# Kernel tuning notes

Hardware: AMD Instinct MI355X
Metric: run time of the kernel (lower is better)

The kernel has to match this reference:

```python
import jax, jax.numpy as jnp
import numpy as np

B, S, HID = 2, 2048, 2048
H, G = 32, 8            # query heads, kv heads
D = HID // H            # head_dim = 64
QPG = H // G            # q heads per kv group = 4


def setup_inputs() -> dict:
    key = jax.random.key(0)
    ks = jax.random.split(key, 5)
    sc = 0.02
    return {
        "x": jax.random.normal(ks[0], (B, S, HID), jnp.float32),
        "Wq": jax.random.normal(ks[1], (HID, HID), jnp.float32) * sc,
        "bq": jnp.zeros((HID,), jnp.float32),
        "Wk": jax.random.normal(ks[2], (HID, G * D), jnp.float32) * sc,
        "bk": jnp.zeros((G * D,), jnp.float32),
        "Wv": jax.random.normal(ks[3], (HID, G * D), jnp.float32) * sc,
        "bv": jnp.zeros((G * D,), jnp.float32),
        "Wo": jax.random.normal(ks[4], (HID, HID), jnp.float32) * sc,
        "bo": jnp.zeros((HID,), jnp.float32),
    }


def reference(x, Wq, bq, Wk, bk, Wv, bv, Wo, bo):
    b, s, _ = x.shape
    # projections (weights stored as [in, out])
    q = (x @ Wq + bq).reshape(b, s, G, QPG, D)      # [b,s,g,p,d]
    k = (x @ Wk + bk).reshape(b, s, G, D)           # [b,s,g,d]
    v = (x @ Wv + bv).reshape(b, s, G, D)
    scale = 1.0 / jnp.sqrt(jnp.asarray(D, x.dtype))
    # grouped attention: repeat_interleave of K/V expressed as shared g axis
    scores = jnp.einsum('bsgpd,btgd->bgpst', q, k) * scale  # [b,g,p,s,t]
    w = jax.nn.softmax(scores, axis=-1)
    o = jnp.einsum('bgpst,btgd->bsgpd', w, v)               # [b,s,g,p,d]
    o = o.reshape(b, s, HID)
    return o @ Wo + bo
```

## Files before the change

### kernel.cpp

```cpp
#include <hip/hip_runtime.h>
#include <hip/hip_bf16.h>


typedef __attribute__((ext_vector_type(8))) short shortx8;
typedef __attribute__((ext_vector_type(4))) float floatx4;

#define SEQ 2048
#define QSC 0.1803368801111204f

#if __has_builtin(__builtin_amdgcn_exp2f)
#define EXP2F(x) __builtin_amdgcn_exp2f(x)
#else
#define EXP2F(x) __expf((x) * 0.6931471805599453f)
#endif

__device__ __forceinline__ unsigned short f2bf(float f) {
  union { float f; unsigned u; } a; a.f = f;
  unsigned u = a.u;
  u += 0x7fffu + ((u >> 16) & 1u);
  return (unsigned short)(u >> 16);
}

__device__ __forceinline__ unsigned cvtpkbf(float lo, float hi) {
  unsigned r;
  asm("v_cvt_pk_bf16_f32 %0, %1, %2" : "=v"(r) : "v"(lo), "v"(hi));
  return r;
}

__device__ __forceinline__ void plswap(unsigned &a, unsigned &b) {
  asm("v_permlane32_swap_b32 %0, %1" : "+v"(a), "+v"(b));
}
__device__ __forceinline__ void pl16swap(unsigned &a, unsigned &b) {
  asm("v_permlane16_swap_b32 %0, %1" : "+v"(a), "+v"(b));
}

__device__ __forceinline__ void gload16(const unsigned short* g, unsigned short* l) {
  __builtin_amdgcn_global_load_lds((const __attribute__((address_space(1))) void*)g,
                                   (__attribute__((address_space(3))) void*)l, 16, 0, 0);
}

__global__ void prep_kernel(const float* __restrict__ x,
                            const float* __restrict__ Wq, const float* __restrict__ Wk,
                            const float* __restrict__ Wv, const float* __restrict__ Wo,
                            const float* __restrict__ bq, const float* __restrict__ bk,
                            const float* __restrict__ bv,
                            unsigned short* __restrict__ WT,
                            unsigned short* __restrict__ WoT,
                            unsigned short* __restrict__ xb,
                            float* __restrict__ bqkv) {
  const int z = blockIdx.z;
  if (z == 4) {
    int fb = blockIdx.y * 64 + blockIdx.x;
    int tid = threadIdx.y * 32 + threadIdx.x;
    int i = fb * 2048 + tid * 8;
    float4 v0 = *(const float4*)(x + i);
    float4 v1 = *(const float4*)(x + i + 4);
    ushort4 o0, o1;
    o0.x = f2bf(v0.x); o0.y = f2bf(v0.y); o0.z = f2bf(v0.z); o0.w = f2bf(v0.w);
    o1.x = f2bf(v1.x); o1.y = f2bf(v1.y); o1.z = f2bf(v1.z); o1.w = f2bf(v1.w);
    *(ushort4*)(xb + i) = o0;
    *(ushort4*)(xb + i + 4) = o1;
    return;
  }
  if (z == 5) {
    int fb = blockIdx.y * 64 + blockIdx.x;
    if (fb >= 12) return;
    int i = fb * 256 + threadIdx.y * 32 + threadIdx.x;
    if (i < 2048) bqkv[i] = bq[i] * QSC;
    else if (i < 2560) bqkv[i] = bk[i - 2048];
    else if (i < 3072) bqkv[i] = bv[i - 2560];
    return;
  }
  const float* W; unsigned short* D; int N; float sc = 1.f;
  if (z == 0)      { W = Wq; D = WT;               N = 2048; sc = QSC; }
  else if (z == 1) { W = Wk; D = WT + 2048 * 2048; N = 512; }
  else if (z == 2) { W = Wv; D = WT + 2560 * 2048; N = 512; }
  else             { W = Wo; D = WoT;              N = 2048; }
  if (blockIdx.x * 32 >= N) return;

  __shared__ float tile[32][33];
  int xx = blockIdx.x * 32 + threadIdx.x;
  int y0 = blockIdx.y * 32;
  for (int i = 0; i < 32; i += 8)
    tile[threadIdx.y + i][threadIdx.x] = W[(size_t)(y0 + threadIdx.y + i) * N + xx];
  __syncthreads();
  int nx = y0 + threadIdx.x;
  int ny = blockIdx.x * 32 + threadIdx.y;
  for (int i = 0; i < 32; i += 8)
    D[(size_t)(ny + i) * 2048 + nx] = f2bf(tile[threadIdx.x][threadIdx.y + i] * sc);
}

template <int MODE>
__global__ __launch_bounds__(256) void gemm_bt(const unsigned short* __restrict__ A,
                                               const unsigned short* __restrict__ BT,
                                               const float* __restrict__ bias,
                                               void* __restrict__ Cout,
                                               unsigned short* __restrict__ Kbuf,
                                               unsigned short* __restrict__ Vt,
                                               int M, int N, int K) {
  __shared__ __align__(16) unsigned short As[128 * 64];
  __shared__ __align__(16) unsigned short Bs[128 * 64];
  const int m0 = blockIdx.x * 128, n0 = blockIdx.y * 128;
  const int tid = threadIdx.x;
  const int lane = tid & 63, wave = tid >> 6;
  const int l15 = lane & 15, quad = lane >> 4;
  const int wm = (wave & 1) * 64, wn = (wave >> 1) * 64;

  const int r8 = lane >> 3;
  const int clog = (lane & 7) ^ r8;
  const unsigned short* aSrc = A + (size_t)(m0 + wave * 32 + r8) * K + clog * 8;
  const unsigned short* bSrc = BT + (size_t)(n0 + wave * 32 + r8) * K + clog * 8;
  unsigned short* aDst = &As[wave * 2048];
  unsigned short* bDst = &Bs[wave * 2048];

  const int s = l15 & 7;
  int aoff[4], boff[4];
#pragma unroll
  for (int i = 0; i < 4; i++) aoff[i] = (wm + i * 16 + l15) * 64 + (quad ^ s) * 8;
#pragma unroll
  for (int j = 0; j < 4; j++) boff[j] = (wn + j * 16 + l15) * 64 + (quad ^ s) * 8;

  floatx4 acc[4][4];
#pragma unroll
  for (int i = 0; i < 4; i++)
#pragma unroll
    for (int j = 0; j < 4; j++)
#pragma unroll
      for (int r = 0; r < 4; r++) acc[i][j][r] = 0.f;

  for (int k0 = 0; k0 < K; k0 += 64) {
    __syncthreads();
#pragma unroll
    for (int j = 0; j < 4; j++) {
      gload16(aSrc + (size_t)j * 8 * K + k0, aDst + j * 512);
      gload16(bSrc + (size_t)j * 8 * K + k0, bDst + j * 512);
    }
    __syncthreads();
    {
      shortx8 af[4], bf[4];
#pragma unroll
      for (int i = 0; i < 4; i++) af[i] = *(const shortx8*)&As[aoff[i]];
#pragma unroll
      for (int j = 0; j < 4; j++) bf[j] = *(const shortx8*)&Bs[boff[j]];
#pragma unroll
      for (int i = 0; i < 4; i++)
#pragma unroll
        for (int j = 0; j < 4; j++)
          acc[i][j] = __builtin_amdgcn_mfma_f32_16x16x32_bf16(af[i], bf[j], acc[i][j], 0, 0, 0);
#pragma unroll
      for (int i = 0; i < 4; i++) af[i] = *(const shortx8*)&As[aoff[i] ^ 32];
#pragma unroll
      for (int j = 0; j < 4; j++) bf[j] = *(const shortx8*)&Bs[boff[j] ^ 32];
#pragma unroll
      for (int i = 0; i < 4; i++)
#pragma unroll
        for (int j = 0; j < 4; j++)
          acc[i][j] = __builtin_amdgcn_mfma_f32_16x16x32_bf16(af[i], bf[j], acc[i][j], 0, 0, 0);
    }
  }

#pragma unroll
  for (int i = 0; i < 4; i++) {
#pragma unroll
    for (int j = 0; j < 4; j++) {
      int col = n0 + wn + j * 16 + l15;
      float bv = bias[col];
#pragma unroll
      for (int r = 0; r < 4; r++) {
        int row = m0 + wm + i * 16 + quad * 4 + r;
        float v = acc[i][j][r] + bv;
        if (MODE == 0) {
          ((float*)Cout)[(size_t)row * N + col] = v;
        } else {
          if (col < 2048) {
            ((unsigned short*)Cout)[(size_t)row * 2048 + col] = f2bf(v);
          } else if (col < 2560) {
            Kbuf[(size_t)row * 512 + (col - 2048)] = f2bf(v);
          } else {
            int g = (col - 2560) >> 6, d = (col - 2560) & 63;
            int b = row >> 11, sidx = row & 2047;
            Vt[(size_t)(((g << 1) | b) * 64 + d) * 2048 + sidx] = f2bf(v);
          }
        }
      }
    }
  }
}

__global__ __launch_bounds__(256, 4) void attn_kernel(const unsigned short* __restrict__ Qb,
                                                      const unsigned short* __restrict__ Kb,
                                                      const unsigned short* __restrict__ Vt,
                                                      unsigned short* __restrict__ O) {
  const int qt = blockIdx.x, g = blockIdx.y, b = blockIdx.z;
  const int tid = threadIdx.x;
  const int lane = tid & 63, wave = tid >> 6;
  const int h = g * 4 + wave;
  const int l15 = lane & 15, quad = lane >> 4;

  __shared__ __align__(16) unsigned short Ks[2][64 * 64];
  __shared__ __align__(16) unsigned short Vs[2][64 * 64];

  shortx8 qf[2][2];
  {
    const unsigned short* qp = Qb + (size_t)(b * SEQ + qt * 32 + l15) * 2048 + h * 64 + quad * 8;
#pragma unroll
    for (int a = 0; a < 2; a++) {
      qf[a][0] = *(const shortx8*)(qp + (size_t)a * 16 * 2048);
      qf[a][1] = *(const shortx8*)(qp + (size_t)a * 16 * 2048 + 32);
    }
  }

  const int r8 = lane >> 3;
  const int clog = (lane & 7) ^ r8;
  const unsigned short* kSrc = Kb + ((size_t)b * SEQ + wave * 16 + r8) * 512 + g * 64 + clog * 8;
  const unsigned short* vSrc = Vt + ((size_t)((g * 2 + b) * 64 + wave * 16 + r8)) * 2048 + clog * 8;

  const int s = l15 & 7;
  int foff[4];
#pragma unroll
  for (int i = 0; i < 4; i++) foff[i] = (i * 16 + l15) * 64 + ((quad ^ s) * 8);

  shortx8 ones;
#pragma unroll
  for (int j = 0; j < 8; j++) ones[j] = (short)0x3F80;

  floatx4 oacc[2][4], lacc[2];
#pragma unroll
  for (int a = 0; a < 2; a++) {
#pragma unroll
    for (int r = 0; r < 4; r++) lacc[a][r] = 0.f;
#pragma unroll
    for (int nd = 0; nd < 4; nd++)
#pragma unroll
      for (int r = 0; r < 4; r++) oacc[a][nd][r] = 0.f;
  }

  {
    unsigned short* kD = &Ks[0][wave * 1024];
    unsigned short* vD = &Vs[0][wave * 1024];
    gload16(kSrc, kD);
    gload16(kSrc + (size_t)8 * 512, kD + 512);
    gload16(vSrc, vD);
    gload16(vSrc + (size_t)8 * 2048, vD + 512);
  }
  __syncthreads();

  for (int it = 0; it < SEQ / 64; it++) {
    const int p = it & 1;
    if (it < SEQ / 64 - 1) {
      const size_t t1 = (size_t)(it + 1) * 64;
      unsigned short* kD = &Ks[p ^ 1][wave * 1024];
      unsigned short* vD = &Vs[p ^ 1][wave * 1024];
      gload16(kSrc + t1 * 512, kD);
      gload16(kSrc + (t1 + 8) * 512, kD + 512);
      gload16(vSrc + t1, vD);
      gload16(vSrc + (size_t)8 * 2048 + t1, vD + 512);
    }

    shortx8 kf[4][2];
#pragma unroll
    for (int i = 0; i < 4; i++) {
      kf[i][0] = *(const shortx8*)&Ks[p][foff[i]];
      kf[i][1] = *(const shortx8*)&Ks[p][foff[i] ^ 32];
    }

    shortx8 pfr[2][2];
#pragma unroll
    for (int a = 0; a < 2; a++) {
      floatx4 sc[4];
      __builtin_amdgcn_s_setprio(1);
#pragma unroll
      for (int i = 0; i < 4; i++) {
        floatx4 c = {0.f, 0.f, 0.f, 0.f};
        c = __builtin_amdgcn_mfma_f32_16x16x32_bf16(kf[i][0], qf[a][0], c, 0, 0, 0);
        c = __builtin_amdgcn_mfma_f32_16x16x32_bf16(kf[i][1], qf[a][1], c, 0, 0, 0);
        sc[i] = c;
      }
      __builtin_amdgcn_s_setprio(0);
      unsigned E00 = cvtpkbf(EXP2F(sc[0][0]), EXP2F(sc[0][1]));
      unsigned E01 = cvtpkbf(EXP2F(sc[0][2]), EXP2F(sc[0][3]));
      unsigned E10 = cvtpkbf(EXP2F(sc[1][0]), EXP2F(sc[1][1]));
      unsigned E11 = cvtpkbf(EXP2F(sc[1][2]), EXP2F(sc[1][3]));
      unsigned E20 = cvtpkbf(EXP2F(sc[2][0]), EXP2F(sc[2][1]));
      unsigned E21 = cvtpkbf(EXP2F(sc[2][2]), EXP2F(sc[2][3]));
      unsigned E30 = cvtpkbf(EXP2F(sc[3][0]), EXP2F(sc[3][1]));
      unsigned E31 = cvtpkbf(EXP2F(sc[3][2]), EXP2F(sc[3][3]));
      plswap(E00, E10); plswap(E01, E11);
      plswap(E20, E30); plswap(E21, E31);
      pl16swap(E00, E10); pl16swap(E01, E11);
      pl16swap(E20, E30); pl16swap(E21, E31);
      union { unsigned u[4]; shortx8 v; } P0, P1;
      P0.u[0] = E00; P0.u[1] = E01; P0.u[2] = E10; P0.u[3] = E11;
      P1.u[0] = E20; P1.u[1] = E21; P1.u[2] = E30; P1.u[3] = E31;
      pfr[a][0] = P0.v;
      pfr[a][1] = P1.v;
    }

    shortx8 vf[4][2];
#pragma unroll
    for (int nd = 0; nd < 4; nd++) {
      vf[nd][0] = *(const shortx8*)&Vs[p][foff[nd]];
      vf[nd][1] = *(const shortx8*)&Vs[p][foff[nd] ^ 32];
    }
#pragma unroll
    for (int a = 0; a < 2; a++) {
#pragma unroll
      for (int ks = 0; ks < 2; ks++) {
        shortx8 pf = pfr[a][ks];
        __builtin_amdgcn_s_setprio(1);
#pragma unroll
        for (int nd = 0; nd < 4; nd++)
          oacc[a][nd] = __builtin_amdgcn_mfma_f32_16x16x32_bf16(vf[nd][ks], pf, oacc[a][nd], 0, 0, 0);
        lacc[a] = __builtin_amdgcn_mfma_f32_16x16x32_bf16(ones, pf, lacc[a], 0, 0, 0);
        __builtin_amdgcn_s_setprio(0);
      }
    }
    __syncthreads();
  }

#pragma unroll
  for (int a = 0; a < 2; a++) {
    float inv = 1.f / lacc[a][0];
    unsigned short* oPtr = O + (size_t)(b * SEQ + qt * 32 + a * 16 + l15) * 2048 + h * 64 + quad * 4;
#pragma unroll
    for (int nd = 0; nd < 4; nd++) {
      uint2 w;
      w.x = (unsigned)f2bf(oacc[a][nd][0] * inv) | ((unsigned)f2bf(oacc[a][nd][1] * inv) << 16);
      w.y = (unsigned)f2bf(oacc[a][nd][2] * inv) | ((unsigned)f2bf(oacc[a][nd][3] * inv) << 16);
      *(uint2*)(oPtr + nd * 16) = w;
    }
  }
}

extern "C" void kernel_launch(void* const* d_in, const int* in_sizes, int n_in,
                              void* d_out, int out_size, void* d_ws, size_t ws_size,
                              hipStream_t stream) {
  const float* x  = (const float*)d_in[0];
  const float* Wq = (const float*)d_in[1];
  const float* bq = (const float*)d_in[2];
  const float* Wk = (const float*)d_in[3];
  const float* bk = (const float*)d_in[4];
  const float* Wv = (const float*)d_in[5];
  const float* bv = (const float*)d_in[6];
  const float* Wo = (const float*)d_in[7];
  const float* bo = (const float*)d_in[8];
  float* out = (float*)d_out;

  char* ws = (char*)d_ws;
  unsigned short* WTall = (unsigned short*)ws;
  unsigned short* WoT   = (unsigned short*)(ws + 12582912);
  float*          bqkv  = (float*)(ws + 20971520);
  unsigned short* xb    = (unsigned short*)(ws + 20987904);
  unsigned short* Qbuf  = (unsigned short*)(ws + 37765120);
  unsigned short* Kbuf  = (unsigned short*)(ws + 54542336);
  unsigned short* Vt    = (unsigned short*)(ws + 58736640);
  unsigned short* Og    = xb;

  prep_kernel<<<dim3(64, 64, 6), dim3(32, 8), 0, stream>>>(
      x, Wq, Wk, Wv, Wo, bq, bk, bv, WTall, WoT, xb, bqkv);

  gemm_bt<2><<<dim3(32, 24), 256, 0, stream>>>(xb, WTall, bqkv, Qbuf, Kbuf, Vt, 4096, 3072, 2048);

  attn_kernel<<<dim3(64, 8, 2), 256, 0, stream>>>(Qbuf, Kbuf, Vt, Og);

  gemm_bt<0><<<dim3(32, 16), 256, 0, stream>>>(Og, WoT, bo, out, nullptr, nullptr, 4096, 2048, 2048);
}
```

Baseline: 304.8 us.

## Double per-block query tile to 64 rows to reuse K/V loads more

```diff
diff --git a/kernel.cpp b/kernel.cpp
--- a/kernel.cpp
+++ b/kernel.cpp
@@ -28,10 +28,10 @@
 }
 
 __device__ __forceinline__ void plswap(unsigned &a, unsigned &b) {
-  asm("v_permlane32_swap_b32 %0, %1" : "+v"(a), "+v"(b));
+  asm("s_nop 1\n\tv_permlane32_swap_b32 %0, %1" : "+v"(a), "+v"(b));
 }
 __device__ __forceinline__ void pl16swap(unsigned &a, unsigned &b) {
-  asm("v_permlane16_swap_b32 %0, %1" : "+v"(a), "+v"(b));
+  asm("s_nop 1\n\tv_permlane16_swap_b32 %0, %1" : "+v"(a), "+v"(b));
 }
 
 __device__ __forceinline__ void gload16(const unsigned short* g, unsigned short* l) {
@@ -187,7 +187,57 @@
   }
 }
 
-__global__ __launch_bounds__(256, 4) void attn_kernel(const unsigned short* __restrict__ Qb,
+__device__ __forceinline__ floatx4 mfma16(const shortx8 &a, const shortx8 &b, floatx4 c) {
+  return __builtin_amdgcn_mfma_f32_16x16x32_bf16(a, b, c, 0, 0, 0);
+}
+
+__device__ __forceinline__ void qk8(const shortx8 (&kf)[4][2], const shortx8 (&qfa)[2],
+                                    floatx4 (&sc)[4]) {
+  __builtin_amdgcn_s_setprio(1);
+#pragma unroll
+  for (int i = 0; i < 4; i++) {
+    floatx4 c = {0.f, 0.f, 0.f, 0.f};
+    c = mfma16(kf[i][0], qfa[0], c);
+    c = mfma16(kf[i][1], qfa[1], c);
+    sc[i] = c;
+  }
+  __builtin_amdgcn_s_setprio(0);
+}
+
+__device__ __forceinline__ void expbfly(const floatx4 (&sc)[4], shortx8 (&pf)[2]) {
+  unsigned E00 = cvtpkbf(EXP2F(sc[0][0]), EXP2F(sc[0][1]));
+  unsigned E01 = cvtpkbf(EXP2F(sc[0][2]), EXP2F(sc[0][3]));
+  unsigned E10 = cvtpkbf(EXP2F(sc[1][0]), EXP2F(sc[1][1]));
+  unsigned E11 = cvtpkbf(EXP2F(sc[1][2]), EXP2F(sc[1][3]));
+  unsigned E20 = cvtpkbf(EXP2F(sc[2][0]), EXP2F(sc[2][1]));
+  unsigned E21 = cvtpkbf(EXP2F(sc[2][2]), EXP2F(sc[2][3]));
+  unsigned E30 = cvtpkbf(EXP2F(sc[3][0]), EXP2F(sc[3][1]));
+  unsigned E31 = cvtpkbf(EXP2F(sc[3][2]), EXP2F(sc[3][3]));
+  plswap(E00, E10); plswap(E01, E11);
+  plswap(E20, E30); plswap(E21, E31);
+  pl16swap(E00, E10); pl16swap(E01, E11);
+  pl16swap(E20, E30); pl16swap(E21, E31);
+  union { unsigned u[4]; shortx8 v; } P0, P1;
+  P0.u[0] = E00; P0.u[1] = E01; P0.u[2] = E10; P0.u[3] = E11;
+  P1.u[0] = E20; P1.u[1] = E21; P1.u[2] = E30; P1.u[3] = E31;
+  pf[0] = P0.v;
+  pf[1] = P1.v;
+}
+
+__device__ __forceinline__ void pv10(const shortx8 (&vf)[4][2], const shortx8 (&pf)[2],
+                                     floatx4 (&oa)[4], floatx4 &la, const shortx8 &ones) {
+#pragma unroll
+  for (int ks = 0; ks < 2; ks++) {
+    __builtin_amdgcn_s_setprio(1);
+#pragma unroll
+    for (int nd = 0; nd < 4; nd++)
+      oa[nd] = mfma16(vf[nd][ks], pf[ks], oa[nd]);
+    la = mfma16(ones, pf[ks], la);
+    __builtin_amdgcn_s_setprio(0);
+  }
+}
+
+__global__ __launch_bounds__(256, 2) void attn_kernel(const unsigned short* __restrict__ Qb,
                                                       const unsigned short* __restrict__ Kb,
                                                       const unsigned short* __restrict__ Vt,
                                                       unsigned short* __restrict__ O) {
@@ -200,11 +250,11 @@
   __shared__ __align__(16) unsigned short Ks[2][64 * 64];
   __shared__ __align__(16) unsigned short Vs[2][64 * 64];
 
-  shortx8 qf[2][2];
+  shortx8 qf[4][2];
   {
-    const unsigned short* qp = Qb + (size_t)(b * SEQ + qt * 32 + l15) * 2048 + h * 64 + quad * 8;
-#pragma unroll
-    for (int a = 0; a < 2; a++) {
+    const unsigned short* qp = Qb + (size_t)(b * SEQ + qt * 64 + l15) * 2048 + h * 64 + quad * 8;
+#pragma unroll
+    for (int a = 0; a < 4; a++) {
       qf[a][0] = *(const shortx8*)(qp + (size_t)a * 16 * 2048);
       qf[a][1] = *(const shortx8*)(qp + (size_t)a * 16 * 2048 + 32);
     }
@@ -224,9 +274,9 @@
 #pragma unroll
   for (int j = 0; j < 8; j++) ones[j] = (short)0x3F80;
 
-  floatx4 oacc[2][4], lacc[2];
-#pragma unroll
-  for (int a = 0; a < 2; a++) {
+  floatx4 oacc[4][4], lacc[4];
+#pragma unroll
+  for (int a = 0; a < 4; a++) {
 #pragma unroll
     for (int r = 0; r < 4; r++) lacc[a][r] = 0.f;
 #pragma unroll
@@ -264,36 +314,12 @@
       kf[i][1] = *(const shortx8*)&Ks[p][foff[i] ^ 32];
     }
 
-    shortx8 pfr[2][2];
-#pragma unroll
-    for (int a = 0; a < 2; a++) {
+    shortx8 pfr[4][2];
+#pragma unroll
+    for (int a = 0; a < 4; a++) {
       floatx4 sc[4];
-      __builtin_amdgcn_s_setprio(1);
-#pragma unroll
-      for (int i = 0; i < 4; i++) {
-        floatx4 c = {0.f, 0.f, 0.f, 0.f};
-        c = __builtin_amdgcn_mfma_f32_16x16x32_bf16(kf[i][0], qf[a][0], c, 0, 0, 0);
-        c = __builtin_amdgcn_mfma_f32_16x16x32_bf16(kf[i][1], qf[a][1], c, 0, 0, 0);
-        sc[i] = c;
-      }
-      __builtin_amdgcn_s_setprio(0);
-      unsigned E00 = cvtpkbf(EXP2F(sc[0][0]), EXP2F(sc[0][1]));
-      unsigned E01 = cvtpkbf(EXP2F(sc[0][2]), EXP2F(sc[0][3]));
-      unsigned E10 = cvtpkbf(EXP2F(sc[1][0]), EXP2F(sc[1][1]));
-      unsigned E11 = cvtpkbf(EXP2F(sc[1][2]), EXP2F(sc[1][3]));
-      unsigned E20 = cvtpkbf(EXP2F(sc[2][0]), EXP2F(sc[2][1]));
-      unsigned E21 = cvtpkbf(EXP2F(sc[2][2]), EXP2F(sc[2][3]));
-      unsigned E30 = cvtpkbf(EXP2F(sc[3][0]), EXP2F(sc[3][1]));
-      unsigned E31 = cvtpkbf(EXP2F(sc[3][2]), EXP2F(sc[3][3]));
-      plswap(E00, E10); plswap(E01, E11);
-      plswap(E20, E30); plswap(E21, E31);
-      pl16swap(E00, E10); pl16swap(E01, E11);
-      pl16swap(E20, E30); pl16swap(E21, E31);
-      union { unsigned u[4]; shortx8 v; } P0, P1;
-      P0.u[0] = E00; P0.u[1] = E01; P0.u[2] = E10; P0.u[3] = E11;
-      P1.u[0] = E20; P1.u[1] = E21; P1.u[2] = E30; P1.u[3] = E31;
-      pfr[a][0] = P0.v;
-      pfr[a][1] = P1.v;
+      qk8(kf, qf[a], sc);
+      expbfly(sc, pfr[a]);
     }
 
     shortx8 vf[4][2];
@@ -303,25 +329,16 @@
       vf[nd][1] = *(const shortx8*)&Vs[p][foff[nd] ^ 32];
     }
 #pragma unroll
-    for (int a = 0; a < 2; a++) {
-#pragma unroll
-      for (int ks = 0; ks < 2; ks++) {
-        shortx8 pf = pfr[a][ks];
-        __builtin_amdgcn_s_setprio(1);
-#pragma unroll
-        for (int nd = 0; nd < 4; nd++)
-          oacc[a][nd] = __builtin_amdgcn_mfma_f32_16x16x32_bf16(vf[nd][ks], pf, oacc[a][nd], 0, 0, 0);
-        lacc[a] = __builtin_amdgcn_mfma_f32_16x16x32_bf16(ones, pf, lacc[a], 0, 0, 0);
-        __builtin_amdgcn_s_setprio(0);
-      }
-    }
+    for (int a = 0; a < 4; a++)
+      pv10(vf, pfr[a], oacc[a], lacc[a], ones);
+
     __syncthreads();
   }
 
 #pragma unroll
-  for (int a = 0; a < 2; a++) {
+  for (int a = 0; a < 4; a++) {
     float inv = 1.f / lacc[a][0];
-    unsigned short* oPtr = O + (size_t)(b * SEQ + qt * 32 + a * 16 + l15) * 2048 + h * 64 + quad * 4;
+    unsigned short* oPtr = O + (size_t)(b * SEQ + qt * 64 + a * 16 + l15) * 2048 + h * 64 + quad * 4;
 #pragma unroll
     for (int nd = 0; nd < 4; nd++) {
       uint2 w;
@@ -361,7 +378,7 @@
 
   gemm_bt<2><<<dim3(32, 24), 256, 0, stream>>>(xb, WTall, bqkv, Qbuf, Kbuf, Vt, 4096, 3072, 2048);
 
-  attn_kernel<<<dim3(64, 8, 2), 256, 0, stream>>>(Qbuf, Kbuf, Vt, Og);
+  attn_kernel<<<dim3(32, 8, 2), 256, 0, stream>>>(Qbuf, Kbuf, Vt, Og);
 
   gemm_bt<0><<<dim3(32, 16), 256, 0, stream>>>(Og, WoT, bo, out, nullptr, nullptr, 4096, 2048, 2048);
 }
```

Result: no change. 302.4 us (-0.8%).
